# Kernel optimization log

Hardware: AMD Instinct MI355X
Metric: run time of the kernel (lower is better)

The kernel has to match this reference:

```python
import jax, jax.numpy as jnp
import numpy as np

N_NODES = 50000
N_EDGES = 600000
HID = 128
N_GRAPHS = 64
SLOPE = 0.2  # PyG GATConv default negative_slope


def gat_conv(x, src, dst, W, a_src, a_dst, b, n_nodes):
    """Single-head PyG-style GATConv with self-loops already included in (src,dst)."""
    xp = x @ W                                  # [N, HID]
    al_s = xp @ a_src                           # [N]
    al_d = xp @ a_dst                           # [N]
    alpha = jax.nn.leaky_relu(al_s[src] + al_d[dst], SLOPE)  # [E+N]
    # segment softmax over edges grouped by destination node
    m = jax.ops.segment_max(alpha, dst, num_segments=n_nodes)
    e = jnp.exp(alpha - m[dst])
    den = jax.ops.segment_sum(e, dst, num_segments=n_nodes)
    coef = e / den[dst]                         # [E+N]
    out = jax.ops.segment_sum(coef[:, None] * xp[src], dst, num_segments=n_nodes)
    return out + b


def setup_inputs() -> dict:
    key = jax.random.key(0)
    ks = jax.random.split(key, 16)
    x = jax.random.normal(ks[0], (N_NODES, 1), dtype=jnp.float32)
    edge_index = jax.random.randint(ks[1], (2, N_EDGES), 0, N_NODES, dtype=jnp.int64)
    batch = jnp.sort(jax.random.randint(ks[2], (N_NODES,), 0, N_GRAPHS, dtype=jnp.int64))

    def glorot(k, shape):
        lim = float(np.sqrt(6.0 / (shape[0] + shape[-1])))
        return jax.random.uniform(k, shape, jnp.float32, -lim, lim)

    params = {}
    dims = [(1, HID), (HID, HID), (HID, HID)]
    for i, (din, dout) in enumerate(dims, start=1):
        params[f"W{i}"] = glorot(ks[2 + 4 * i - 3], (din, dout))
        params[f"as{i}"] = glorot(ks[2 + 4 * i - 2], (dout,))
        params[f"ad{i}"] = glorot(ks[2 + 4 * i - 1], (dout,))
        params[f"b{i}"] = jnp.zeros((dout,), jnp.float32)
    params["Wlin"] = glorot(ks[15], (HID, 2))
    params["blin"] = jnp.zeros((2,), jnp.float32)
    return {"x": x, "edge_index": edge_index, "batch": batch, **params}


def reference(x, edge_index, batch,
              W1, as1, ad1, b1,
              W2, as2, ad2, b2,
              W3, as3, ad3, b3,
              Wlin, blin):
    n = x.shape[0]
    # add self loops (PyG default add_self_loops=True)
    loop = jnp.arange(n, dtype=edge_index.dtype)
    src = jnp.concatenate([edge_index[0], loop])
    dst = jnp.concatenate([edge_index[1], loop])

    h = jax.nn.relu(gat_conv(x, src, dst, W1, as1, ad1, b1, n))
    h = jax.nn.relu(gat_conv(h, src, dst, W2, as2, ad2, b2, n))
    h = jax.nn.relu(gat_conv(h, src, dst, W3, as3, ad3, b3, n))

    # global mean pool per graph
    sums = jax.ops.segment_sum(h, batch, num_segments=N_GRAPHS)
    cnt = jax.ops.segment_sum(jnp.ones((n,), h.dtype), batch, num_segments=N_GRAPHS)
    pooled = sums / jnp.maximum(cnt, 1.0)[:, None]
    # dropout is inactive in eval mode
    return jax.nn.sigmoid(pooled @ Wlin + blin)
```

## Files before the change

kernel.cpp:

```cpp
#include <hip/hip_runtime.h>
#include <hip/hip_bf16.h>
#include <math.h>

#define NNODES 50000
#define NEDGES 600000
#define ETOT   (NEDGES + NNODES)
#define HID    128
#define NGRAPH 64
#define SLOPE  0.2f
#define EB1    2540
#define SLOTS  64

typedef unsigned int  uint32;
typedef unsigned short ushort16;
typedef __attribute__((ext_vector_type(8))) short short8;
typedef __attribute__((ext_vector_type(4))) float floatx4;
typedef __attribute__((ext_vector_type(2))) float floatx2;

__device__ __forceinline__ unsigned short f2bf(float f) {
    unsigned u = __float_as_uint(f);
    unsigned r = (u + 0x7fff + ((u >> 16) & 1)) >> 16;
    return (unsigned short)r;
}
__device__ __forceinline__ uint32 pack_bf2(float a, float b) {
    return (uint32)f2bf(a) | ((uint32)f2bf(b) << 16);
}
__device__ __forceinline__ float bf_lo(uint32 u) { return __uint_as_float(u << 16); }
__device__ __forceinline__ float bf_hi(uint32 u) { return __uint_as_float(u & 0xffff0000u); }

__device__ __forceinline__ floatx2 unpack_fp8x2(unsigned short u) {
    return __builtin_amdgcn_cvt_pk_f32_fp8((int)(unsigned)u, false);
}

__device__ __forceinline__ float wave_sum(float v) {
    #pragma unroll
    for (int m = 32; m >= 1; m >>= 1) v += __shfl_xor(v, m, 64);
    return v;
}
__device__ __forceinline__ float wave_max(float v) {
    #pragma unroll
    for (int m = 32; m >= 1; m >>= 1) v = fmaxf(v, __shfl_xor(v, m, 64));
    return v;
}

__global__ void k_histprep(const int* __restrict__ ei, int* __restrict__ cnt,
                           int* __restrict__ ssrc,
                           const float* __restrict__ W2, const float* __restrict__ as2,
                           const float* __restrict__ ad2,
                           const float* __restrict__ W3, const float* __restrict__ as3,
                           const float* __restrict__ ad3,
                           ushort16* __restrict__ wswz2, ushort16* __restrict__ wswz3,
                           float* __restrict__ was2, float* __restrict__ wad2,
                           float* __restrict__ was3, float* __restrict__ wad3,
                           const float* __restrict__ W1, const float* __restrict__ as1,
                           const float* __restrict__ ad1, float* __restrict__ cbuf) {
    int blk = blockIdx.x;
    int t = threadIdx.x;
    if (blk < 8 * EB1) {
        int xcd = blk & 7;
        int chunk = blk >> 3;
        int e = chunk * 256 + t;
        if (e < ETOT) {
            int d = (e < NEDGES) ? ei[NEDGES + e] : (e - NEDGES);
            uint32 rng = (uint32)(((unsigned long long)(uint32)d * 687196ull) >> 32);
            if (rng == (uint32)xcd) {
                int s = (e < NEDGES) ? ei[e] : d;
                int r = atomicAdd(&cnt[d], 1);
                if (r < SLOTS) ssrc[(d << 6) + r] = s;
            }
        }
    } else if (blk < 8 * EB1 + 32) {
        int b = blk - 8 * EB1;
        int lane = t & 63, wid = t >> 6;
        int k = b * 4 + wid;
        {
            float a2l = as2[lane], a2h = as2[lane + 64];
            float d2l = ad2[lane], d2h = ad2[lane + 64];
            float a3l = as3[lane], a3h = as3[lane + 64];
            float d3l = ad3[lane], d3h = ad3[lane + 64];
            float w2l = W2[k * 128 + lane], w2h = W2[k * 128 + 64 + lane];
            float w3l = W3[k * 128 + lane], w3h = W3[k * 128 + 64 + lane];
            float s2 = wave_sum(w2l * a2l + w2h * a2h);
            float t2 = wave_sum(w2l * d2l + w2h * d2h);
            float s3 = wave_sum(w3l * a3l + w3h * a3h);
            float t3 = wave_sum(w3l * d3l + w3h * d3h);
            if (lane == 0) { was2[k] = s2; wad2[k] = t2; was3[k] = s3; wad3[k] = t3; }
        }
        int gid = b * 256 + t;
        {
            int off = gid * 2;
            int j = off & 7, r = off >> 3;
            int nn = r & 15; r >>= 4;
            int q = r & 3;   r >>= 2;
            int ct = r & 7;  int kc = r >> 3;
            int kk = kc * 32 + q * 8 + j;
            int n  = ct * 16 + nn;
            uint32 u2 = pack_bf2(W2[kk * 128 + n], W2[(kk + 1) * 128 + n]);
            uint32 u3 = pack_bf2(W3[kk * 128 + n], W3[(kk + 1) * 128 + n]);
            ((uint32*)wswz2)[gid] = u2;
            ((uint32*)wswz3)[gid] = u3;
        }
    } else {
        if (t < 64) {
            int l = t;
            float w0 = W1[l], w1 = W1[l + 64];
            float ds = w0 * as1[l] + w1 * as1[l + 64];
            float dd = w0 * ad1[l] + w1 * ad1[l + 64];
            ds = wave_sum(ds); dd = wave_sum(dd);
            if (l == 0) { cbuf[0] = ds; cbuf[1] = dd; }
        }
    }
}

__launch_bounds__(256)
__global__ void k_gemm(const ushort16* __restrict__ H,
                       const float* __restrict__ xsrc, const int* __restrict__ cnt,
                       const int* __restrict__ ssrc, const float* __restrict__ cbuf,
                       const float* __restrict__ W1, const float* __restrict__ b1,
                       const ushort16* __restrict__ wswz, unsigned char* __restrict__ Cq,
                       const float* __restrict__ was, const float* __restrict__ wad,
                       float* __restrict__ als, float* __restrict__ ald, int nrows) {
    __shared__ ushort16 Wl[16384];
    __shared__ float wasl[128], wadl[128];
    __shared__ float sdl[64];
    int t = threadIdx.x;
    int lane = t & 63, wid = t >> 6;
    int nn = lane & 15, q = lane >> 4;
    int row0 = blockIdx.x * 64;
    {
        const uint4* src = (const uint4*)wswz;
        uint4* dst = (uint4*)Wl;
        #pragma unroll
        for (int i = 0; i < 8; i++) dst[t + i * 256] = src[t + i * 256];
        if (t < 128) { wasl[t] = was[t]; wadl[t] = wad[t]; }
    }
    if (xsrc != nullptr) {
        int r = t >> 2, p = t & 3;
        int d = row0 + r;
        float sdv = 0.f;
        if (d < nrows) {
            float cs = cbuf[0], cd = cbuf[1];
            float ald_ = xsrc[d] * cd;
            int deg = cnt[d]; if (deg > SLOTS) deg = SLOTS;
            float mymax = -3.4e38f;
            for (int k = p; k < deg; k += 4) {
                float a = fmaf(xsrc[ssrc[(d << 6) + k]], cs, ald_);
                a = a > 0.f ? a : SLOPE * a;
                mymax = fmaxf(mymax, a);
            }
            mymax = fmaxf(mymax, __shfl_xor(mymax, 1, 64));
            mymax = fmaxf(mymax, __shfl_xor(mymax, 2, 64));
            float den = 0.f, num = 0.f;
            for (int k = p; k < deg; k += 4) {
                float xs = xsrc[ssrc[(d << 6) + k]];
                float a = fmaf(xs, cs, ald_);
                a = a > 0.f ? a : SLOPE * a;
                float w = __expf(a - mymax);
                den += w; num += w * xs;
            }
            den += __shfl_xor(den, 1, 64); den += __shfl_xor(den, 2, 64);
            num += __shfl_xor(num, 1, 64); num += __shfl_xor(num, 2, 64);
            sdv = num / den;
        }
        if (p == 0) sdl[r] = sdv;
    }
    __syncthreads();
    int row = row0 + wid * 16 + nn;
    int rowc = row < nrows ? row : nrows - 1;
    floatx4 acc[8];
    #pragma unroll
    for (int ct = 0; ct < 8; ct++) acc[ct] = (floatx4){0.f, 0.f, 0.f, 0.f};
    float ps = 0.f, pd = 0.f;

    #pragma unroll
    for (int kc = 0; kc < 4; kc++) {
        short8 af;
        float hf[8];
        if (xsrc == nullptr) {
            uint4 av = *(const uint4*)(H + (size_t)rowc * 128 + kc * 32 + q * 8);
            af = *(short8*)&av;
            #pragma unroll
            for (int j = 0; j < 8; j++)
                hf[j] = __uint_as_float(((uint32)(unsigned short)af[j]) << 16);
        } else {
            float s = sdl[wid * 16 + nn];
            int kk = kc * 32 + q * 8;
            float4 w1a = *(const float4*)(W1 + kk), w1b = *(const float4*)(W1 + kk + 4);
            float4 b1a = *(const float4*)(b1 + kk), b1b = *(const float4*)(b1 + kk + 4);
            hf[0] = fmaxf(fmaf(s, w1a.x, b1a.x), 0.f);
            hf[1] = fmaxf(fmaf(s, w1a.y, b1a.y), 0.f);
            hf[2] = fmaxf(fmaf(s, w1a.z, b1a.z), 0.f);
            hf[3] = fmaxf(fmaf(s, w1a.w, b1a.w), 0.f);
            hf[4] = fmaxf(fmaf(s, w1b.x, b1b.x), 0.f);
            hf[5] = fmaxf(fmaf(s, w1b.y, b1b.y), 0.f);
            hf[6] = fmaxf(fmaf(s, w1b.z, b1b.z), 0.f);
            hf[7] = fmaxf(fmaf(s, w1b.w, b1b.w), 0.f);
            uint4 av = make_uint4(pack_bf2(hf[0], hf[1]), pack_bf2(hf[2], hf[3]),
                                  pack_bf2(hf[4], hf[5]), pack_bf2(hf[6], hf[7]));
            af = *(short8*)&av;
        }
        const float* wp = wasl + kc * 32 + q * 8;
        const float* dp = wadl + kc * 32 + q * 8;
        #pragma unroll
        for (int j = 0; j < 8; j++) { ps = fmaf(hf[j], wp[j], ps); pd = fmaf(hf[j], dp[j], pd); }
        #pragma unroll
        for (int ct = 0; ct < 8; ct++) {
            int boff = (((kc * 8 + ct) * 4 + q) * 16 + nn) * 8;
            uint4 bv = *(const uint4*)(Wl + boff);
            short8 bfr = *(short8*)&bv;
            acc[ct] = __builtin_amdgcn_mfma_f32_16x16x32_bf16(af, bfr, acc[ct], 0, 0, 0);
        }
    }
    ps += __shfl_xor(ps, 16, 64); ps += __shfl_xor(ps, 32, 64);
    pd += __shfl_xor(pd, 16, 64); pd += __shfl_xor(pd, 32, 64);
    if (q == 0 && row < nrows) { als[row] = ps; ald[row] = pd; }
    int rbase = row0 + wid * 16 + q * 4;
    #pragma unroll
    for (int reg = 0; reg < 4; reg++) {
        int r = rbase + reg;
        if (r < nrows) {
            unsigned char* cp = Cq + (size_t)r * 128 + nn;
            #pragma unroll
            for (int ct = 0; ct < 8; ct++) {
                float v = acc[ct][reg];
                cp[ct * 16] = (unsigned char)(__builtin_amdgcn_cvt_pk_fp8_f32(v, v, 0, false) & 0xff);
            }
        }
    }
}

__launch_bounds__(256)
__global__ void k_agg(const unsigned char* __restrict__ xp, const float* __restrict__ als,
                      const float* __restrict__ ald_, const int* __restrict__ cnt,
                      const int* __restrict__ ssrc, const float* __restrict__ b,
                      ushort16* __restrict__ hout) {
    __shared__ float2 swbuf[4][64];
    int wid = threadIdx.x >> 6, lane = threadIdx.x & 63;
    int d = blockIdx.x * 4 + wid;
    if (d >= NNODES) return;
    int deg = cnt[d]; if (deg > SLOTS) deg = SLOTS;
    float adv = ald_[d];
    float2 acc = make_float2(0.f, 0.f);

    int s_l = 0;
    float a_l = -3.4e38f;
    if (lane < deg) {
        s_l = ssrc[(d << 6) + lane];
        float a = als[s_l] + adv;
        a_l = a > 0.f ? a : SLOPE * a;
    }
    float m = wave_max(a_l);
    float w_l = (lane < deg) ? __expf(a_l - m) : 0.f;
    float den = wave_sum(w_l);
    swbuf[wid][lane] = make_float2(w_l, __int_as_float(s_l));
    int k = 0;
    int n8 = deg & ~7;
    for (; k < n8; k += 8) {
        float2 p[8];
        unsigned short u[8];
        #pragma unroll
        for (int j = 0; j < 8; j++) p[j] = swbuf[wid][k + j];
        #pragma unroll
        for (int j = 0; j < 8; j++)
            u[j] = *((const unsigned short*)(xp + (size_t)__float_as_int(p[j].y) * 128) + lane);
        #pragma unroll
        for (int j = 0; j < 8; j++) {
            floatx2 v = unpack_fp8x2(u[j]);
            acc.x = fmaf(p[j].x, v.x, acc.x);
            acc.y = fmaf(p[j].x, v.y, acc.y);
        }
    }
    for (; k + 4 <= deg; k += 4) {
        float2 p0 = swbuf[wid][k + 0];
        float2 p1 = swbuf[wid][k + 1];
        float2 p2 = swbuf[wid][k + 2];
        float2 p3 = swbuf[wid][k + 3];
        unsigned short u0 = *((const unsigned short*)(xp + (size_t)__float_as_int(p0.y) * 128) + lane);
        unsigned short u1 = *((const unsigned short*)(xp + (size_t)__float_as_int(p1.y) * 128) + lane);
        unsigned short u2 = *((const unsigned short*)(xp + (size_t)__float_as_int(p2.y) * 128) + lane);
        unsigned short u3 = *((const unsigned short*)(xp + (size_t)__float_as_int(p3.y) * 128) + lane);
        floatx2 v0 = unpack_fp8x2(u0), v1 = unpack_fp8x2(u1);
        floatx2 v2 = unpack_fp8x2(u2), v3 = unpack_fp8x2(u3);
        acc.x = fmaf(p0.x, v0.x, acc.x); acc.y = fmaf(p0.x, v0.y, acc.y);
        acc.x = fmaf(p1.x, v1.x, acc.x); acc.y = fmaf(p1.x, v1.y, acc.y);
        acc.x = fmaf(p2.x, v2.x, acc.x); acc.y = fmaf(p2.x, v2.y, acc.y);
        acc.x = fmaf(p3.x, v3.x, acc.x); acc.y = fmaf(p3.x, v3.y, acc.y);
    }
    for (; k < deg; k++) {
        float2 p = swbuf[wid][k];
        unsigned short uu = *((const unsigned short*)(xp + (size_t)__float_as_int(p.y) * 128) + lane);
        floatx2 v = unpack_fp8x2(uu);
        acc.x = fmaf(p.x, v.x, acc.x); acc.y = fmaf(p.x, v.y, acc.y);
    }
    float inv = 1.f / den;
    float2 bb = *(const float2*)(b + lane * 2);
    float ox = fmaxf(fmaf(acc.x, inv, bb.x), 0.f);
    float oy = fmaxf(fmaf(acc.y, inv, bb.y), 0.f);
    *((uint32*)(hout + (size_t)d * 128) + lane) = pack_bf2(ox, oy);
}

#define PNW 64
__global__ void k_pool(const ushort16* __restrict__ h, const int* __restrict__ batch,
                       float* __restrict__ pool, float* __restrict__ gcnt) {
    int wid = threadIdx.x >> 6, lane = threadIdx.x & 63;
    int base = (blockIdx.x * 4 + wid) * PNW;
    if (base >= NNODES) return;
    int end = base + PNW; if (end > NNODES) end = NNODES;
    float2 acc = make_float2(0.f, 0.f);
    float cnt = 0.f;
    int curg = batch[base];
    for (int i = base; i < end; i++) {
        int g = batch[i];
        if (g != curg) {
            atomicAdd(&pool[curg * 128 + lane * 2], acc.x);
            atomicAdd(&pool[curg * 128 + lane * 2 + 1], acc.y);
            if (lane == 0) atomicAdd(&gcnt[curg], cnt);
            curg = g; acc = make_float2(0.f, 0.f); cnt = 0.f;
        }
        uint32 u = *((const uint32*)(h + (size_t)i * 128) + lane);
        acc.x += bf_lo(u); acc.y += bf_hi(u); cnt += 1.f;
    }
    atomicAdd(&pool[curg * 128 + lane * 2], acc.x);
    atomicAdd(&pool[curg * 128 + lane * 2 + 1], acc.y);
    if (lane == 0) atomicAdd(&gcnt[curg], cnt);
}

__global__ void k_final(const float* __restrict__ pool, const float* __restrict__ gcnt,
                        const float* __restrict__ Wlin, const float* __restrict__ blin,
                        float* __restrict__ out) {
    int t = threadIdx.x;
    int g = t >> 1, k = t & 1;
    float c = fmaxf(gcnt[g], 1.f);
    float acc = 0.f;
    for (int j = 0; j < 128; j++) acc += pool[g * 128 + j] * Wlin[j * 2 + k];
    acc = acc / c + blin[k];
    out[g * 2 + k] = 1.f / (1.f + __expf(-acc));
}

extern "C" void kernel_launch(void* const* d_in, const int* in_sizes, int n_in,
                              void* d_out, int out_size, void* d_ws, size_t ws_size,
                              hipStream_t stream) {
    const float* x    = (const float*)d_in[0];
    const int*   ei   = (const int*)d_in[1];
    const int*   batch= (const int*)d_in[2];
    const float* W1   = (const float*)d_in[3];
    const float* as1  = (const float*)d_in[4];
    const float* ad1  = (const float*)d_in[5];
    const float* b1   = (const float*)d_in[6];
    const float* W2   = (const float*)d_in[7];
    const float* as2  = (const float*)d_in[8];
    const float* ad2  = (const float*)d_in[9];
    const float* b2   = (const float*)d_in[10];
    const float* W3   = (const float*)d_in[11];
    const float* as3  = (const float*)d_in[12];
    const float* ad3  = (const float*)d_in[13];
    const float* b3   = (const float*)d_in[14];
    const float* Wlin = (const float*)d_in[15];
    const float* blin = (const float*)d_in[16];
    float* out = (float*)d_out;

    char* ws = (char*)d_ws;
    size_t off = 0;
    ushort16* bufA = (ushort16*)(ws + off); off += (size_t)NNODES * HID * 2;
    unsigned char* bufB = (unsigned char*)(ws + off); off += (size_t)NNODES * HID;
    float* als    = (float*)(ws + off); off += NNODES * 4;
    float* ald    = (float*)(ws + off); off += NNODES * 4;
    int*   ssrc   = (int*)(ws + off);   off += (size_t)NNODES * SLOTS * 4;
    ushort16* wswz2 = (ushort16*)(ws + off); off += 16384 * 2;
    ushort16* wswz3 = (ushort16*)(ws + off); off += 16384 * 2;
    float* was2   = (float*)(ws + off); off += 128 * 4;
    float* wad2   = (float*)(ws + off); off += 128 * 4;
    float* was3   = (float*)(ws + off); off += 128 * 4;
    float* wad3   = (float*)(ws + off); off += 128 * 4;
    char*  zbase  = ws + off;
    int*   cnt    = (int*)(ws + off);   off += NNODES * 4;
    float* pool   = (float*)(ws + off); off += NGRAPH * HID * 4;
    float* gcnt   = (float*)(ws + off); off += 64 * 4;
    size_t zbytes = (size_t)((char*)(ws + off) - zbase);
    float* cbuf   = (float*)(ws + off); off += 64;

    hipMemsetAsync(zbase, 0, zbytes, stream);

    k_histprep<<<8 * EB1 + 33, 256, 0, stream>>>(ei, cnt, ssrc,
                                                 W2, as2, ad2, W3, as3, ad3,
                                                 wswz2, wswz3, was2, wad2, was3, wad3,
                                                 W1, as1, ad1, cbuf);

    k_gemm<<<(NNODES + 63) / 64, 256, 0, stream>>>(nullptr, x, cnt, ssrc, cbuf, W1, b1,
                                                   wswz2, bufB, was2, wad2, als, ald, NNODES);
    k_agg<<<(NNODES + 3) / 4, 256, 0, stream>>>(bufB, als, ald, cnt, ssrc, b2, bufA);

    k_gemm<<<(NNODES + 63) / 64, 256, 0, stream>>>(bufA, nullptr, nullptr, nullptr, nullptr,
                                                   nullptr, nullptr,
                                                   wswz3, bufB, was3, wad3, als, ald, NNODES);
    k_agg<<<(NNODES + 3) / 4, 256, 0, stream>>>(bufB, als, ald, cnt, ssrc, b3, bufA);

    k_pool<<<(NNODES + 4 * PNW - 1) / (4 * PNW), 256, 0, stream>>>(bufA, batch, pool, gcnt);
    k_final<<<1, 128, 0, stream>>>(pool, gcnt, Wlin, blin, out);
}
```

Measured before the change: 238.2 us.

## Fuse layer-2 aggregation into layer-3 GEMM and fold pooling and head into layer-3 aggregation

Layer-2 aggregation now runs inside the layer-3 GEMM kernel. Each block aggregates its 64 rows into swizzled shared memory as bf16 and then runs the MFMA projection straight from LDS, so the bf16 hidden matrix never round-trips through global memory. The layer-3 aggregation is fused with mean pooling, and a last-block ticket counter runs the final linear and sigmoid, which removes the separate pool and final kernels and two launches. The catch is lower parallelism: aggregation goes from 4 nodes per block to 16 nodes per wave, which may expose gather latency. The fused GEMM also uses a larger LDS footprint, which limits occupancy.

After: 337.9 us. 41.8% more time.

```diff
diff --git a/kernel.cpp b/kernel.cpp
--- a/kernel.cpp
+++ b/kernel.cpp
@@ -10,6 +10,7 @@
 #define SLOPE  0.2f
 #define EB1    2540
 #define SLOTS  64
+#define NB     782
 
 typedef unsigned int  uint32;
 typedef unsigned short ushort16;
@@ -41,6 +42,70 @@
     #pragma unroll
     for (int m = 32; m >= 1; m >>= 1) v = fmaxf(v, __shfl_xor(v, m, 64));
     return v;
+}
+
+__device__ __forceinline__ void agg_node(int d, int lane,
+        const unsigned char* __restrict__ xp, const float* __restrict__ alsv,
+        const float* __restrict__ aldv, const int* __restrict__ cnt,
+        const int* __restrict__ ssrc, const float* __restrict__ bvec,
+        float2* swrow, float& ox, float& oy) {
+    int deg = cnt[d]; if (deg > SLOTS) deg = SLOTS;
+    float adv = aldv[d];
+    float2 acc = make_float2(0.f, 0.f);
+    int s_l = 0;
+    float a_l = -3.4e38f;
+    if (lane < deg) {
+        s_l = ssrc[(d << 6) + lane];
+        float a = alsv[s_l] + adv;
+        a_l = a > 0.f ? a : SLOPE * a;
+    }
+    float m = wave_max(a_l);
+    float w_l = (lane < deg) ? __expf(a_l - m) : 0.f;
+    float den = wave_sum(w_l);
+    swrow[lane] = make_float2(w_l, __int_as_float(s_l));
+    int k = 0;
+    int n8 = deg & ~7;
+    for (; k < n8; k += 8) {
+        float2 p[8];
+        unsigned short u[8];
+        #pragma unroll
+        for (int j = 0; j < 8; j++) p[j] = swrow[k + j];
+        #pragma unroll
+        for (int j = 0; j < 8; j++)
+            u[j] = *((const unsigned short*)(xp + (size_t)__float_as_int(p[j].y) * 128) + lane);
+        #pragma unroll
+        for (int j = 0; j < 8; j++) {
+            floatx2 v = unpack_fp8x2(u[j]);
+            acc.x = fmaf(p[j].x, v.x, acc.x);
+            acc.y = fmaf(p[j].x, v.y, acc.y);
+        }
+    }
+    for (; k + 4 <= deg; k += 4) {
+        float2 p0 = swrow[k + 0];
+        float2 p1 = swrow[k + 1];
+        float2 p2 = swrow[k + 2];
+        float2 p3 = swrow[k + 3];
+        unsigned short u0 = *((const unsigned short*)(xp + (size_t)__float_as_int(p0.y) * 128) + lane);
+        unsigned short u1 = *((const unsigned short*)(xp + (size_t)__float_as_int(p1.y) * 128) + lane);
+        unsigned short u2 = *((const unsigned short*)(xp + (size_t)__float_as_int(p2.y) * 128) + lane);
+        unsigned short u3 = *((const unsigned short*)(xp + (size_t)__float_as_int(p3.y) * 128) + lane);
+        floatx2 v0 = unpack_fp8x2(u0), v1 = unpack_fp8x2(u1);
+        floatx2 v2 = unpack_fp8x2(u2), v3 = unpack_fp8x2(u3);
+        acc.x = fmaf(p0.x, v0.x, acc.x); acc.y = fmaf(p0.x, v0.y, acc.y);
+        acc.x = fmaf(p1.x, v1.x, acc.x); acc.y = fmaf(p1.x, v1.y, acc.y);
+        acc.x = fmaf(p2.x, v2.x, acc.x); acc.y = fmaf(p2.x, v2.y, acc.y);
+        acc.x = fmaf(p3.x, v3.x, acc.x); acc.y = fmaf(p3.x, v3.y, acc.y);
+    }
+    for (; k < deg; k++) {
+        float2 p = swrow[k];
+        unsigned short uu = *((const unsigned short*)(xp + (size_t)__float_as_int(p.y) * 128) + lane);
+        floatx2 v = unpack_fp8x2(uu);
+        acc.x = fmaf(p.x, v.x, acc.x); acc.y = fmaf(p.x, v.y, acc.y);
+    }
+    float inv = 1.f / den;
+    float2 bb = *(const float2*)(bvec + lane * 2);
+    ox = fmaxf(fmaf(acc.x, inv, bb.x), 0.f);
+    oy = fmaxf(fmaf(acc.y, inv, bb.y), 0.f);
 }
 
 __global__ void k_histprep(const int* __restrict__ ei, int* __restrict__ cnt,
@@ -113,13 +178,12 @@
 }
 
 __launch_bounds__(256)
-__global__ void k_gemm(const ushort16* __restrict__ H,
-                       const float* __restrict__ xsrc, const int* __restrict__ cnt,
-                       const int* __restrict__ ssrc, const float* __restrict__ cbuf,
-                       const float* __restrict__ W1, const float* __restrict__ b1,
-                       const ushort16* __restrict__ wswz, unsigned char* __restrict__ Cq,
-                       const float* __restrict__ was, const float* __restrict__ wad,
-                       float* __restrict__ als, float* __restrict__ ald, int nrows) {
+__global__ void k_gemmL2(const float* __restrict__ xsrc, const int* __restrict__ cnt,
+                         const int* __restrict__ ssrc, const float* __restrict__ cbuf,
+                         const float* __restrict__ W1, const float* __restrict__ b1,
+                         const ushort16* __restrict__ wswz, unsigned char* __restrict__ Cq,
+                         const float* __restrict__ was, const float* __restrict__ wad,
+                         float* __restrict__ als, float* __restrict__ ald) {
     __shared__ ushort16 Wl[16384];
     __shared__ float wasl[128], wadl[128];
     __shared__ float sdl[64];
@@ -134,11 +198,11 @@
         for (int i = 0; i < 8; i++) dst[t + i * 256] = src[t + i * 256];
         if (t < 128) { wasl[t] = was[t]; wadl[t] = wad[t]; }
     }
-    if (xsrc != nullptr) {
+    {
         int r = t >> 2, p = t & 3;
         int d = row0 + r;
         float sdv = 0.f;
-        if (d < nrows) {
+        if (d < NNODES) {
             float cs = cbuf[0], cd = cbuf[1];
             float ald_ = xsrc[d] * cd;
             int deg = cnt[d]; if (deg > SLOTS) deg = SLOTS;
@@ -166,7 +230,6 @@
     }
     __syncthreads();
     int row = row0 + wid * 16 + nn;
-    int rowc = row < nrows ? row : nrows - 1;
     floatx4 acc[8];
     #pragma unroll
     for (int ct = 0; ct < 8; ct++) acc[ct] = (floatx4){0.f, 0.f, 0.f, 0.f};
@@ -176,13 +239,7 @@
     for (int kc = 0; kc < 4; kc++) {
         short8 af;
         float hf[8];
-        if (xsrc == nullptr) {
-            uint4 av = *(const uint4*)(H + (size_t)rowc * 128 + kc * 32 + q * 8);
-            af = *(short8*)&av;
-            #pragma unroll
-            for (int j = 0; j < 8; j++)
-                hf[j] = __uint_as_float(((uint32)(unsigned short)af[j]) << 16);
-        } else {
+        {
             float s = sdl[wid * 16 + nn];
             int kk = kc * 32 + q * 8;
             float4 w1a = *(const float4*)(W1 + kk), w1b = *(const float4*)(W1 + kk + 4);
@@ -213,12 +270,12 @@
     }
     ps += __shfl_xor(ps, 16, 64); ps += __shfl_xor(ps, 32, 64);
     pd += __shfl_xor(pd, 16, 64); pd += __shfl_xor(pd, 32, 64);
-    if (q == 0 && row < nrows) { als[row] = ps; ald[row] = pd; }
+    if (q == 0 && row < NNODES) { als[row] = ps; ald[row] = pd; }
     int rbase = row0 + wid * 16 + q * 4;
     #pragma unroll
     for (int reg = 0; reg < 4; reg++) {
         int r = rbase + reg;
-        if (r < nrows) {
+        if (r < NNODES) {
             unsigned char* cp = Cq + (size_t)r * 128 + nn;
             #pragma unroll
             for (int ct = 0; ct < 8; ct++) {
@@ -229,112 +286,141 @@
     }
 }
 
+__launch_bounds__(256, 3)
+__global__ void k_aggGemm(const unsigned char* __restrict__ xp,
+                          const float* __restrict__ als2, const float* __restrict__ ald2,
+                          const int* __restrict__ cnt, const int* __restrict__ ssrc,
+                          const float* __restrict__ b2, const int* __restrict__ batchdummy,
+                          const ushort16* __restrict__ wswz,
+                          const float* __restrict__ was, const float* __restrict__ wad,
+                          unsigned char* __restrict__ Cq,
+                          float* __restrict__ als3, float* __restrict__ ald3) {
+    __shared__ ushort16 Wl[16384];
+    __shared__ uint32 hl[64 * 64];
+    __shared__ float wasl[128], wadl[128];
+    __shared__ float2 swbuf[4][64];
+    int t = threadIdx.x;
+    int lane = t & 63, wid = t >> 6;
+    int nn = lane & 15, q = lane >> 4;
+    int row0 = blockIdx.x * 64;
+    {
+        const uint4* src = (const uint4*)wswz;
+        uint4* dst = (uint4*)Wl;
+        #pragma unroll
+        for (int i = 0; i < 8; i++) dst[t + i * 256] = src[t + i * 256];
+        if (t < 128) { wasl[t] = was[t]; wadl[t] = wad[t]; }
+    }
+    for (int i = 0; i < 16; i++) {
+        int r = wid * 16 + i;
+        int d = row0 + r;
+        if (d < NNODES) {
+            float ox, oy;
+            agg_node(d, lane, xp, als2, ald2, cnt, ssrc, b2, swbuf[wid], ox, oy);
+            hl[r * 64 + (lane ^ ((r & 15) << 2))] = pack_bf2(ox, oy);
+        }
+    }
+    __syncthreads();
+    int row = row0 + wid * 16 + nn;
+    int rA = wid * 16 + nn;
+    floatx4 acc[8];
+    #pragma unroll
+    for (int ct = 0; ct < 8; ct++) acc[ct] = (floatx4){0.f, 0.f, 0.f, 0.f};
+    float ps = 0.f, pd = 0.f;
+    #pragma unroll
+    for (int kc = 0; kc < 4; kc++) {
+        uint4 av = *(const uint4*)&hl[rA * 64 + ((kc * 16 + q * 4) ^ ((rA & 15) << 2))];
+        short8 af = *(short8*)&av;
+        float hf[8];
+        #pragma unroll
+        for (int j = 0; j < 8; j++)
+            hf[j] = __uint_as_float(((uint32)(unsigned short)af[j]) << 16);
+        const float* wp = wasl + kc * 32 + q * 8;
+        const float* dp = wadl + kc * 32 + q * 8;
+        #pragma unroll
+        for (int j = 0; j < 8; j++) { ps = fmaf(hf[j], wp[j], ps); pd = fmaf(hf[j], dp[j], pd); }
+        #pragma unroll
+        for (int ct = 0; ct < 8; ct++) {
+            int boff = (((kc * 8 + ct) * 4 + q) * 16 + nn) * 8;
+            uint4 bv = *(const uint4*)(Wl + boff);
+            short8 bfr = *(short8*)&bv;
+            acc[ct] = __builtin_amdgcn_mfma_f32_16x16x32_bf16(af, bfr, acc[ct], 0, 0, 0);
+        }
+    }
+    ps += __shfl_xor(ps, 16, 64); ps += __shfl_xor(ps, 32, 64);
+    pd += __shfl_xor(pd, 16, 64); pd += __shfl_xor(pd, 32, 64);
+    if (q == 0 && row < NNODES) { als3[row] = ps; ald3[row] = pd; }
+    int rbase = row0 + wid * 16 + q * 4;
+    #pragma unroll
+    for (int reg = 0; reg < 4; reg++) {
+        int r = rbase + reg;
+        if (r < NNODES) {
+            unsigned char* cp = Cq + (size_t)r * 128 + nn;
+            #pragma unroll
+            for (int ct = 0; ct < 8; ct++) {
+                float v = acc[ct][reg];
+                cp[ct * 16] = (unsigned char)(__builtin_amdgcn_cvt_pk_fp8_f32(v, v, 0, false) & 0xff);
+            }
+        }
+    }
+}
+
 __launch_bounds__(256)
-__global__ void k_agg(const unsigned char* __restrict__ xp, const float* __restrict__ als,
-                      const float* __restrict__ ald_, const int* __restrict__ cnt,
-                      const int* __restrict__ ssrc, const float* __restrict__ b,
-                      ushort16* __restrict__ hout) {
+__global__ void k_aggPoolFinal(const unsigned char* __restrict__ xp,
+        const float* __restrict__ als, const float* __restrict__ ald_,
+        const int* __restrict__ cnt, const int* __restrict__ ssrc,
+        const float* __restrict__ b, const int* __restrict__ batch,
+        float* __restrict__ pool, float* __restrict__ gcnt,
+        int* __restrict__ tick,
+        const float* __restrict__ Wlin, const float* __restrict__ blin,
+        float* __restrict__ out) {
     __shared__ float2 swbuf[4][64];
-    int wid = threadIdx.x >> 6, lane = threadIdx.x & 63;
-    int d = blockIdx.x * 4 + wid;
-    if (d >= NNODES) return;
-    int deg = cnt[d]; if (deg > SLOTS) deg = SLOTS;
-    float adv = ald_[d];
+    __shared__ int lastflag;
+    int t = threadIdx.x, wid = t >> 6, lane = t & 63;
+    int wave = blockIdx.x * 4 + wid;
+    int d0 = wave * 16;
+    int d1 = d0 + 16; if (d1 > NNODES) d1 = NNODES;
     float2 acc = make_float2(0.f, 0.f);
-
-    int s_l = 0;
-    float a_l = -3.4e38f;
-    if (lane < deg) {
-        s_l = ssrc[(d << 6) + lane];
-        float a = als[s_l] + adv;
-        a_l = a > 0.f ? a : SLOPE * a;
-    }
-    float m = wave_max(a_l);
-    float w_l = (lane < deg) ? __expf(a_l - m) : 0.f;
-    float den = wave_sum(w_l);
-    swbuf[wid][lane] = make_float2(w_l, __int_as_float(s_l));
-    int k = 0;
-    int n8 = deg & ~7;
-    for (; k < n8; k += 8) {
-        float2 p[8];
-        unsigned short u[8];
-        #pragma unroll
-        for (int j = 0; j < 8; j++) p[j] = swbuf[wid][k + j];
-        #pragma unroll
-        for (int j = 0; j < 8; j++)
-            u[j] = *((const unsigned short*)(xp + (size_t)__float_as_int(p[j].y) * 128) + lane);
-        #pragma unroll
-        for (int j = 0; j < 8; j++) {
-            floatx2 v = unpack_fp8x2(u[j]);
-            acc.x = fmaf(p[j].x, v.x, acc.x);
-            acc.y = fmaf(p[j].x, v.y, acc.y);
-        }
-    }
-    for (; k + 4 <= deg; k += 4) {
-        float2 p0 = swbuf[wid][k + 0];
-        float2 p1 = swbuf[wid][k + 1];
-        float2 p2 = swbuf[wid][k + 2];
-        float2 p3 = swbuf[wid][k + 3];
-        unsigned short u0 = *((const unsigned short*)(xp + (size_t)__float_as_int(p0.y) * 128) + lane);
-        unsigned short u1 = *((const unsigned short*)(xp + (size_t)__float_as_int(p1.y) * 128) + lane);
-        unsigned short u2 = *((const unsigned short*)(xp + (size_t)__float_as_int(p2.y) * 128) + lane);
-        unsigned short u3 = *((const unsigned short*)(xp + (size_t)__float_as_int(p3.y) * 128) + lane);
-        floatx2 v0 = unpack_fp8x2(u0), v1 = unpack_fp8x2(u1);
-        floatx2 v2 = unpack_fp8x2(u2), v3 = unpack_fp8x2(u3);
-        acc.x = fmaf(p0.x, v0.x, acc.x); acc.y = fmaf(p0.x, v0.y, acc.y);
-        acc.x = fmaf(p1.x, v1.x, acc.x); acc.y = fmaf(p1.x, v1.y, acc.y);
-        acc.x = fmaf(p2.x, v2.x, acc.x); acc.y = fmaf(p2.x, v2.y, acc.y);
-        acc.x = fmaf(p3.x, v3.x, acc.x); acc.y = fmaf(p3.x, v3.y, acc.y);
-    }
-    for (; k < deg; k++) {
-        float2 p = swbuf[wid][k];
-        unsigned short uu = *((const unsigned short*)(xp + (size_t)__float_as_int(p.y) * 128) + lane);
-        floatx2 v = unpack_fp8x2(uu);
-        acc.x = fmaf(p.x, v.x, acc.x); acc.y = fmaf(p.x, v.y, acc.y);
-    }
-    float inv = 1.f / den;
-    float2 bb = *(const float2*)(b + lane * 2);
-    float ox = fmaxf(fmaf(acc.x, inv, bb.x), 0.f);
-    float oy = fmaxf(fmaf(acc.y, inv, bb.y), 0.f);
-    *((uint32*)(hout + (size_t)d * 128) + lane) = pack_bf2(ox, oy);
-}
-
-#define PNW 64
-__global__ void k_pool(const ushort16* __restrict__ h, const int* __restrict__ batch,
-                       float* __restrict__ pool, float* __restrict__ gcnt) {
-    int wid = threadIdx.x >> 6, lane = threadIdx.x & 63;
-    int base = (blockIdx.x * 4 + wid) * PNW;
-    if (base >= NNODES) return;
-    int end = base + PNW; if (end > NNODES) end = NNODES;
-    float2 acc = make_float2(0.f, 0.f);
-    float cnt = 0.f;
-    int curg = batch[base];
-    for (int i = base; i < end; i++) {
-        int g = batch[i];
+    float cf = 0.f;
+    int curg = -1;
+    for (int d = d0; d < d1; d++) {
+        float ox, oy;
+        agg_node(d, lane, xp, als, ald_, cnt, ssrc, b, swbuf[wid], ox, oy);
+        int g = batch[d];
         if (g != curg) {
-            atomicAdd(&pool[curg * 128 + lane * 2], acc.x);
-            atomicAdd(&pool[curg * 128 + lane * 2 + 1], acc.y);
-            if (lane == 0) atomicAdd(&gcnt[curg], cnt);
-            curg = g; acc = make_float2(0.f, 0.f); cnt = 0.f;
-        }
-        uint32 u = *((const uint32*)(h + (size_t)i * 128) + lane);
-        acc.x += bf_lo(u); acc.y += bf_hi(u); cnt += 1.f;
-    }
-    atomicAdd(&pool[curg * 128 + lane * 2], acc.x);
-    atomicAdd(&pool[curg * 128 + lane * 2 + 1], acc.y);
-    if (lane == 0) atomicAdd(&gcnt[curg], cnt);
-}
-
-__global__ void k_final(const float* __restrict__ pool, const float* __restrict__ gcnt,
-                        const float* __restrict__ Wlin, const float* __restrict__ blin,
-                        float* __restrict__ out) {
-    int t = threadIdx.x;
-    int g = t >> 1, k = t & 1;
-    float c = fmaxf(gcnt[g], 1.f);
-    float acc = 0.f;
-    for (int j = 0; j < 128; j++) acc += pool[g * 128 + j] * Wlin[j * 2 + k];
-    acc = acc / c + blin[k];
-    out[g * 2 + k] = 1.f / (1.f + __expf(-acc));
+            if (curg >= 0) {
+                atomicAdd(&pool[curg * 128 + lane * 2], acc.x);
+                atomicAdd(&pool[curg * 128 + lane * 2 + 1], acc.y);
+                if (lane == 0) atomicAdd(&gcnt[curg], cf);
+            }
+            curg = g; acc = make_float2(0.f, 0.f); cf = 0.f;
+        }
+        acc.x += ox; acc.y += oy; cf += 1.f;
+    }
+    if (curg >= 0) {
+        atomicAdd(&pool[curg * 128 + lane * 2], acc.x);
+        atomicAdd(&pool[curg * 128 + lane * 2 + 1], acc.y);
+        if (lane == 0) atomicAdd(&gcnt[curg], cf);
+    }
+    __threadfence();
+    __syncthreads();
+    if (t == 0) {
+        int old = __hip_atomic_fetch_add(tick, 1, __ATOMIC_ACQ_REL, __HIP_MEMORY_SCOPE_AGENT);
+        lastflag = (old == NB - 1) ? 1 : 0;
+    }
+    __syncthreads();
+    if (lastflag && t < 128) {
+        int g = t >> 1, k = t & 1;
+        float c = __hip_atomic_load(&gcnt[g], __ATOMIC_RELAXED, __HIP_MEMORY_SCOPE_AGENT);
+        c = fmaxf(c, 1.f);
+        float a2 = 0.f;
+        for (int j = 0; j < 128; j++) {
+            float pv = __hip_atomic_load(&pool[g * 128 + j], __ATOMIC_RELAXED,
+                                         __HIP_MEMORY_SCOPE_AGENT);
+            a2 += pv * Wlin[j * 2 + k];
+        }
+        a2 = a2 / c + blin[k];
+        out[g * 2 + k] = 1.f / (1.f + __expf(-a2));
+    }
 }
 
 extern "C" void kernel_launch(void* const* d_in, const int* in_sizes, int n_in,
@@ -361,10 +447,12 @@
 
     char* ws = (char*)d_ws;
     size_t off = 0;
-    ushort16* bufA = (ushort16*)(ws + off); off += (size_t)NNODES * HID * 2;
-    unsigned char* bufB = (unsigned char*)(ws + off); off += (size_t)NNODES * HID;
+    unsigned char* bufB  = (unsigned char*)(ws + off); off += (size_t)NNODES * HID;
+    unsigned char* bufB2 = (unsigned char*)(ws + off); off += (size_t)NNODES * HID;
     float* als    = (float*)(ws + off); off += NNODES * 4;
     float* ald    = (float*)(ws + off); off += NNODES * 4;
+    float* als3   = (float*)(ws + off); off += NNODES * 4;
+    float* ald3   = (float*)(ws + off); off += NNODES * 4;
     int*   ssrc   = (int*)(ws + off);   off += (size_t)NNODES * SLOTS * 4;
     ushort16* wswz2 = (ushort16*)(ws + off); off += 16384 * 2;
     ushort16* wswz3 = (ushort16*)(ws + off); off += 16384 * 2;
@@ -376,6 +464,7 @@
     int*   cnt    = (int*)(ws + off);   off += NNODES * 4;
     float* pool   = (float*)(ws + off); off += NGRAPH * HID * 4;
     float* gcnt   = (float*)(ws + off); off += 64 * 4;
+    int*   tick   = (int*)(ws + off);   off += 64;
     size_t zbytes = (size_t)((char*)(ws + off) - zbase);
     float* cbuf   = (float*)(ws + off); off += 64;
 
@@ -386,15 +475,12 @@
                                                  wswz2, wswz3, was2, wad2, was3, wad3,
                                                  W1, as1, ad1, cbuf);
 
-    k_gemm<<<(NNODES + 63) / 64, 256, 0, stream>>>(nullptr, x, cnt, ssrc, cbuf, W1, b1,
-                                                   wswz2, bufB, was2, wad2, als, ald, NNODES);
-    k_agg<<<(NNODES + 3) / 4, 256, 0, stream>>>(bufB, als, ald, cnt, ssrc, b2, bufA);
-
-    k_gemm<<<(NNODES + 63) / 64, 256, 0, stream>>>(bufA, nullptr, nullptr, nullptr, nullptr,
-                                                   nullptr, nullptr,
-                                                   wswz3, bufB, was3, wad3, als, ald, NNODES);
-    k_agg<<<(NNODES + 3) / 4, 256, 0, stream>>>(bufB, als, ald, cnt, ssrc, b3, bufA);
-
-    k_pool<<<(NNODES + 4 * PNW - 1) / (4 * PNW), 256, 0, stream>>>(bufA, batch, pool, gcnt);
-    k_final<<<1, 128, 0, stream>>>(pool, gcnt, Wlin, blin, out);
-}
+    k_gemmL2<<<NB, 256, 0, stream>>>(x, cnt, ssrc, cbuf, W1, b1,
+                                     wswz2, bufB, was2, wad2, als, ald);
+
+    k_aggGemm<<<NB, 256, 0, stream>>>(bufB, als, ald, cnt, ssrc, b2, batch,
+                                      wswz3, was3, wad3, bufB2, als3, ald3);
+
+    k_aggPoolFinal<<<NB, 256, 0, stream>>>(bufB2, als3, ald3, cnt, ssrc, b3, batch,
+                                           pool, gcnt, tick, Wlin, blin, out);
+}
```

## Drop XCD-partitioned histogram and fuse pool with final via last-block ticket

Applied to the files above, without the earlier changes.

The edge-bucketing kernel no longer launches eight copies of every edge chunk, one per XCD, each filtering by destination range. It now launches a single pass where each thread does its atomic insert directly, cutting redundant edge reads and block count but losing the XCD-local L2 placement of the atomics on cnt. The pool and final kernels are merged: each block atomically bumps a ticket, and the last block computes the linear layer and sigmoid, removing one kernel launch. The gemm grid sizes are now written as named constants with the same values.

After: 269.0 us. 12.9% more time.

```diff
diff --git a/kernel.cpp b/kernel.cpp
--- a/kernel.cpp
+++ b/kernel.cpp
@@ -10,6 +10,9 @@
 #define SLOPE  0.2f
 #define EB1    2540
 #define SLOTS  64
+#define NB     782
+#define PNW    64
+#define NPB    196
 
 typedef unsigned int  uint32;
 typedef unsigned short ushort16;
@@ -56,21 +59,16 @@
                            const float* __restrict__ ad1, float* __restrict__ cbuf) {
     int blk = blockIdx.x;
     int t = threadIdx.x;
-    if (blk < 8 * EB1) {
-        int xcd = blk & 7;
-        int chunk = blk >> 3;
-        int e = chunk * 256 + t;
+    if (blk < EB1) {
+        int e = blk * 256 + t;
         if (e < ETOT) {
             int d = (e < NEDGES) ? ei[NEDGES + e] : (e - NEDGES);
-            uint32 rng = (uint32)(((unsigned long long)(uint32)d * 687196ull) >> 32);
-            if (rng == (uint32)xcd) {
-                int s = (e < NEDGES) ? ei[e] : d;
-                int r = atomicAdd(&cnt[d], 1);
-                if (r < SLOTS) ssrc[(d << 6) + r] = s;
-            }
-        }
-    } else if (blk < 8 * EB1 + 32) {
-        int b = blk - 8 * EB1;
+            int s = (e < NEDGES) ? ei[e] : d;
+            int r = atomicAdd(&cnt[d], 1);
+            if (r < SLOTS) ssrc[(d << 6) + r] = s;
+        }
+    } else if (blk < EB1 + 32) {
+        int b = blk - EB1;
         int lane = t & 63, wid = t >> 6;
         int k = b * 4 + wid;
         {
@@ -299,42 +297,55 @@
     *((uint32*)(hout + (size_t)d * 128) + lane) = pack_bf2(ox, oy);
 }
 
-#define PNW 64
-__global__ void k_pool(const ushort16* __restrict__ h, const int* __restrict__ batch,
-                       float* __restrict__ pool, float* __restrict__ gcnt) {
+__global__ void k_poolFinal(const ushort16* __restrict__ h, const int* __restrict__ batch,
+                            float* __restrict__ pool, float* __restrict__ gcnt,
+                            int* __restrict__ tick,
+                            const float* __restrict__ Wlin, const float* __restrict__ blin,
+                            float* __restrict__ out) {
+    __shared__ int lastflag;
     int wid = threadIdx.x >> 6, lane = threadIdx.x & 63;
     int base = (blockIdx.x * 4 + wid) * PNW;
-    if (base >= NNODES) return;
-    int end = base + PNW; if (end > NNODES) end = NNODES;
-    float2 acc = make_float2(0.f, 0.f);
-    float cnt = 0.f;
-    int curg = batch[base];
-    for (int i = base; i < end; i++) {
-        int g = batch[i];
-        if (g != curg) {
-            atomicAdd(&pool[curg * 128 + lane * 2], acc.x);
-            atomicAdd(&pool[curg * 128 + lane * 2 + 1], acc.y);
-            if (lane == 0) atomicAdd(&gcnt[curg], cnt);
-            curg = g; acc = make_float2(0.f, 0.f); cnt = 0.f;
-        }
-        uint32 u = *((const uint32*)(h + (size_t)i * 128) + lane);
-        acc.x += bf_lo(u); acc.y += bf_hi(u); cnt += 1.f;
-    }
-    atomicAdd(&pool[curg * 128 + lane * 2], acc.x);
-    atomicAdd(&pool[curg * 128 + lane * 2 + 1], acc.y);
-    if (lane == 0) atomicAdd(&gcnt[curg], cnt);
-}
-
-__global__ void k_final(const float* __restrict__ pool, const float* __restrict__ gcnt,
-                        const float* __restrict__ Wlin, const float* __restrict__ blin,
-                        float* __restrict__ out) {
-    int t = threadIdx.x;
-    int g = t >> 1, k = t & 1;
-    float c = fmaxf(gcnt[g], 1.f);
-    float acc = 0.f;
-    for (int j = 0; j < 128; j++) acc += pool[g * 128 + j] * Wlin[j * 2 + k];
-    acc = acc / c + blin[k];
-    out[g * 2 + k] = 1.f / (1.f + __expf(-acc));
+    if (base < NNODES) {
+        int end = base + PNW; if (end > NNODES) end = NNODES;
+        float2 acc = make_float2(0.f, 0.f);
+        float cf = 0.f;
+        int curg = batch[base];
+        for (int i = base; i < end; i++) {
+            int g = batch[i];
+            if (g != curg) {
+                atomicAdd(&pool[curg * 128 + lane * 2], acc.x);
+                atomicAdd(&pool[curg * 128 + lane * 2 + 1], acc.y);
+                if (lane == 0) atomicAdd(&gcnt[curg], cf);
+                curg = g; acc = make_float2(0.f, 0.f); cf = 0.f;
+            }
+            uint32 u = *((const uint32*)(h + (size_t)i * 128) + lane);
+            acc.x += bf_lo(u); acc.y += bf_hi(u); cf += 1.f;
+        }
+        atomicAdd(&pool[curg * 128 + lane * 2], acc.x);
+        atomicAdd(&pool[curg * 128 + lane * 2 + 1], acc.y);
+        if (lane == 0) atomicAdd(&gcnt[curg], cf);
+    }
+    __threadfence();
+    __syncthreads();
+    if (threadIdx.x == 0) {
+        int old = __hip_atomic_fetch_add(tick, 1, __ATOMIC_ACQ_REL, __HIP_MEMORY_SCOPE_AGENT);
+        lastflag = (old == NPB - 1) ? 1 : 0;
+    }
+    __syncthreads();
+    if (lastflag && threadIdx.x < 128) {
+        int t = threadIdx.x;
+        int g = t >> 1, k = t & 1;
+        float c = __hip_atomic_load(&gcnt[g], __ATOMIC_RELAXED, __HIP_MEMORY_SCOPE_AGENT);
+        c = fmaxf(c, 1.f);
+        float a2 = 0.f;
+        for (int j = 0; j < 128; j++) {
+            float pv = __hip_atomic_load(&pool[g * 128 + j], __ATOMIC_RELAXED,
+                                         __HIP_MEMORY_SCOPE_AGENT);
+            a2 += pv * Wlin[j * 2 + k];
+        }
+        a2 = a2 / c + blin[k];
+        out[g * 2 + k] = 1.f / (1.f + __expf(-a2));
+    }
 }
 
 extern "C" void kernel_launch(void* const* d_in, const int* in_sizes, int n_in,
@@ -376,25 +387,25 @@
     int*   cnt    = (int*)(ws + off);   off += NNODES * 4;
     float* pool   = (float*)(ws + off); off += NGRAPH * HID * 4;
     float* gcnt   = (float*)(ws + off); off += 64 * 4;
+    int*   tick   = (int*)(ws + off);   off += 64;
     size_t zbytes = (size_t)((char*)(ws + off) - zbase);
     float* cbuf   = (float*)(ws + off); off += 64;
 
     hipMemsetAsync(zbase, 0, zbytes, stream);
 
-    k_histprep<<<8 * EB1 + 33, 256, 0, stream>>>(ei, cnt, ssrc,
-                                                 W2, as2, ad2, W3, as3, ad3,
-                                                 wswz2, wswz3, was2, wad2, was3, wad3,
-                                                 W1, as1, ad1, cbuf);
-
-    k_gemm<<<(NNODES + 63) / 64, 256, 0, stream>>>(nullptr, x, cnt, ssrc, cbuf, W1, b1,
-                                                   wswz2, bufB, was2, wad2, als, ald, NNODES);
+    k_histprep<<<EB1 + 33, 256, 0, stream>>>(ei, cnt, ssrc,
+                                             W2, as2, ad2, W3, as3, ad3,
+                                             wswz2, wswz3, was2, wad2, was3, wad3,
+                                             W1, as1, ad1, cbuf);
+
+    k_gemm<<<NB, 256, 0, stream>>>(nullptr, x, cnt, ssrc, cbuf, W1, b1,
+                                   wswz2, bufB, was2, wad2, als, ald, NNODES);
     k_agg<<<(NNODES + 3) / 4, 256, 0, stream>>>(bufB, als, ald, cnt, ssrc, b2, bufA);
 
-    k_gemm<<<(NNODES + 63) / 64, 256, 0, stream>>>(bufA, nullptr, nullptr, nullptr, nullptr,
-                                                   nullptr, nullptr,
-                                                   wswz3, bufB, was3, wad3, als, ald, NNODES);
+    k_gemm<<<NB, 256, 0, stream>>>(bufA, nullptr, nullptr, nullptr, nullptr,
+                                   nullptr, nullptr,
+                                   wswz3, bufB, was3, wad3, als, ald, NNODES);
     k_agg<<<(NNODES + 3) / 4, 256, 0, stream>>>(bufB, als, ald, cnt, ssrc, b3, bufA);
 
-    k_pool<<<(NNODES + 4 * PNW - 1) / (4 * PNW), 256, 0, stream>>>(bufA, batch, pool, gcnt);
-    k_final<<<1, 128, 0, stream>>>(pool, gcnt, Wlin, blin, out);
-}
+    k_poolFinal<<<NPB, 256, 0, stream>>>(bufA, batch, pool, gcnt, tick, Wlin, blin, out);
+}
```
